# Kernel optimization log

Measured on AMD Instinct MI355X. Metric: run time of the kernel, lower is better.

## Reference

```python
import jax, jax.numpy as jnp
import numpy as np

B, S, E, H = 4, 4096, 512, 64


def setup_inputs() -> dict:
    key = jax.random.key(0)
    ks = jax.random.split(key, 6)
    query = jax.random.normal(ks[0], (B, S, E), dtype=jnp.float32)
    key_t = jax.random.normal(ks[1], (B, S, E), dtype=jnp.float32)
    value = jax.random.normal(ks[2], (B, S, E), dtype=jnp.float32)
    # nn.Linear weights are [out, in] = [H, E]; biases [H]
    Wq = jax.random.normal(ks[3], (H, E), dtype=jnp.float32) * 0.02
    Wk = jax.random.normal(ks[4], (H, E), dtype=jnp.float32) * 0.02
    Wv = jax.random.normal(ks[5], (H, E), dtype=jnp.float32) * 0.02
    bq = jnp.zeros((H,), jnp.float32)
    bk = jnp.zeros((H,), jnp.float32)
    bv = jnp.zeros((H,), jnp.float32)
    # causal mask, broadcast over batch; masked_fill where mask == 0
    mask = jnp.tril(jnp.ones((1, S, S), dtype=jnp.bool_))
    return {"query": query, "key": key_t, "value": value,
            "Wq": Wq, "bq": bq, "Wk": Wk, "bk": bk, "Wv": Wv, "bv": bv,
            "mask": mask}


def reference(query, key, value, Wq, bq, Wk, bk, Wv, bv, mask):
    # Bug-faithful: d_k is the LAST dim of the *input* query, i.e. embed_dim
    d_k = query.shape[-1]
    q = jnp.einsum('bse,he->bsh', query, Wq) + bq   # [B,S,H]
    k = jnp.einsum('bse,he->bsh', key, Wk) + bk     # [B,S,H]
    v = jnp.einsum('bse,he->bsh', value, Wv) + bv   # [B,S,H]
    scores = jnp.einsum('bqh,bkh->bqk', q, k) / jnp.sqrt(jnp.float32(d_k))  # [B,S,S]
    scores = jnp.where(mask, scores, -jnp.inf)
    weights = jax.nn.softmax(scores, axis=-1)
    # dropout_rate = 0.0 -> Dropout is identity
    out = jnp.einsum('bqk,bkh->bqh', weights, v)    # [B,S,H]
    return out
```

## Files before the change

### kernel.cpp

```cpp
#include <hip/hip_runtime.h>
#include <hip/hip_bf16.h>
#include <math.h>

typedef unsigned short u16;
typedef unsigned int   u32;
typedef __attribute__((ext_vector_type(8)))  short bf16x8_t;
typedef __attribute__((ext_vector_type(4)))  float f32x4_t;
typedef __attribute__((ext_vector_type(16))) float f32x16_t;
typedef __attribute__((ext_vector_type(4)))  int   i32x4_t;
typedef __attribute__((ext_vector_type(2)))  u32   u32x2_t;

#define SEQ 4096
#define EMB 512
#define HD  64
#define NBATCH 4
#define C2 0.063758718f

#define NPAIR 136
#define SLOTS (NBATCH * NPAIR * 8)

__device__ __forceinline__ u16 to_bf(float f) {
    __hip_bfloat16 h = __float2bfloat16(f);
    return __builtin_bit_cast(u16, h);
}

__device__ __forceinline__ void stage16(const u16* g, u16* l) {
    __builtin_amdgcn_global_load_lds(
        (const __attribute__((address_space(1))) void*)g,
        (__attribute__((address_space(3))) void*)l, 16, 0, 0);
}

__global__ __launch_bounds__(256)
void proj_kernel(const float* __restrict__ q_in, const float* __restrict__ k_in,
                 const float* __restrict__ v_in,
                 const float* __restrict__ Wq, const float* __restrict__ bq,
                 const float* __restrict__ Wk, const float* __restrict__ bk,
                 const float* __restrict__ Wv, const float* __restrict__ bv,
                 u16* __restrict__ outQ, u16* __restrict__ outK,
                 u16* __restrict__ outVT)
{
    const int z = blockIdx.y;
    const float* in   = (z == 0) ? q_in : (z == 1) ? k_in : v_in;
    const float* W    = (z == 0) ? Wq   : (z == 1) ? Wk   : Wv;
    const float* bias = (z == 0) ? bq   : (z == 1) ? bk   : bv;

    __shared__ u16 A_lds[64][72];
    __shared__ u16 B_lds[64][72];

    const int tid  = threadIdx.x;
    const int lane = tid & 63;
    const int w    = tid >> 6;
    const int l15  = lane & 15;
    const int lg   = lane >> 4;
    const int g0   = blockIdx.x * 64;

    f32x4_t acc[4];
    #pragma unroll
    for (int i = 0; i < 4; ++i)
        #pragma unroll
        for (int j = 0; j < 4; ++j) acc[i][j] = 0.f;

    const int r   = tid >> 2;
    const int seg = tid & 3;

    for (int ec = 0; ec < EMB / 64; ++ec) {
        __syncthreads();
        {
            const float* srcA = in + (size_t)(g0 + r) * EMB + ec * 64 + seg * 16;
            const float* srcB = W  + (size_t)r        * EMB + ec * 64 + seg * 16;
            u16 ta[16], tb[16];
            #pragma unroll
            for (int u = 0; u < 4; ++u) {
                f32x4_t fa = *reinterpret_cast<const f32x4_t*>(srcA + 4 * u);
                f32x4_t fb = *reinterpret_cast<const f32x4_t*>(srcB + 4 * u);
                #pragma unroll
                for (int q = 0; q < 4; ++q) {
                    ta[4 * u + q] = to_bf(fa[q]);
                    tb[4 * u + q] = to_bf(fb[q]);
                }
            }
            *reinterpret_cast<i32x4_t*>(&A_lds[r][seg * 16 + 0]) = *reinterpret_cast<i32x4_t*>(&ta[0]);
            *reinterpret_cast<i32x4_t*>(&A_lds[r][seg * 16 + 8]) = *reinterpret_cast<i32x4_t*>(&ta[8]);
            *reinterpret_cast<i32x4_t*>(&B_lds[r][seg * 16 + 0]) = *reinterpret_cast<i32x4_t*>(&tb[0]);
            *reinterpret_cast<i32x4_t*>(&B_lds[r][seg * 16 + 8]) = *reinterpret_cast<i32x4_t*>(&tb[8]);
        }
        __syncthreads();
        #pragma unroll
        for (int ks = 0; ks < 2; ++ks) {
            bf16x8_t a = *reinterpret_cast<const bf16x8_t*>(&A_lds[w * 16 + l15][ks * 32 + 8 * lg]);
            #pragma unroll
            for (int kn = 0; kn < 4; ++kn) {
                bf16x8_t b = *reinterpret_cast<const bf16x8_t*>(&B_lds[kn * 16 + l15][ks * 32 + 8 * lg]);
                acc[kn] = __builtin_amdgcn_mfma_f32_16x16x32_bf16(a, b, acc[kn], 0, 0, 0);
            }
        }
    }

    #pragma unroll
    for (int kn = 0; kn < 4; ++kn) {
        const int col = kn * 16 + l15;
        const float bb = bias[col];
        #pragma unroll
        for (int j = 0; j < 4; ++j) {
            const int grow = g0 + w * 16 + lg * 4 + j;
            const u16 val = to_bf(acc[kn][j] + bb);
            if (z == 0) {
                outQ[(size_t)grow * HD + col] = val;
            } else if (z == 1) {
                outK[(size_t)grow * HD + col] = val;
            } else {
                const int b = grow >> 12, s = grow & (SEQ - 1);
                outVT[((size_t)(b * HD + col)) * SEQ + s] = val;
            }
        }
    }
}

__global__ __launch_bounds__(512, 4)
void attn8_kernel(const u16* __restrict__ Q, const u16* __restrict__ K,
                  const u16* __restrict__ VT,
                  u16* __restrict__ partO, float* __restrict__ partL)
{
    __shared__ u16 Kt[2][64 * 64];
    __shared__ u16 Vt[2][64 * 64];
    __shared__ u16 Pt[8][32 * 64];

    const int tid  = threadIdx.x;
    const int w    = tid >> 6;
    const int lane = tid & 63;
    const int q31  = lane & 31;
    const int half = lane >> 5;

    const int b = blockIdx.y;
    const int y = blockIdx.x;
    int g = 0;
    while ((g + 1) * (g + 2) / 2 <= y) ++g;
    const int c = y - g * (g + 1) / 2;

    const int R0   = 256 * g + 32 * w;
    const int q_g  = R0 + q31;
    const int nt_w = 4 * g + (w >> 1) + 1;
    const int t0   = 4 * c, t1 = 4 * c + 4;

    const u16* Kb  = K  + (size_t)b * SEQ * HD;
    const u16* VTb = VT + (size_t)b * HD * SEQ;

    const int srow = w * 8 + (lane >> 3);
    const int schk = (lane & 7) ^ ((lane >> 3) & 7);

    bf16x8_t qf0, qf1, qf2, qf3;
    {
        const u16* qp = Q + ((size_t)b * SEQ + q_g) * HD + 8 * half;
        qf0 = *(const bf16x8_t*)(qp + 0);
        qf1 = *(const bf16x8_t*)(qp + 16);
        qf2 = *(const bf16x8_t*)(qp + 32);
        qf3 = *(const bf16x8_t*)(qp + 48);
    }

    f32x16_t acc0, acc1;
    #pragma unroll
    for (int i = 0; i < 16; ++i) { acc0[i] = 0.f; acc1[i] = 0.f; }
    float lsum = 0.f;

    auto STAGE = [&](int u, int t) {
        stage16(&Kb[((size_t)(t * 64 + srow)) * HD + schk * 8], &Kt[u][w * 512]);
        stage16(&VTb[(size_t)srow * SEQ + t * 64 + schk * 8],   &Vt[u][w * 512]);
    };

    STAGE(0, t0);
    asm volatile("s_waitcnt vmcnt(0)" ::: "memory");
    __syncthreads();

    for (int t = t0; t < t1; ++t) {
        const int u = (t - t0) & 1;
        if (t + 1 < t1) STAGE(u ^ 1, t + 1);
        if (t < nt_w) {
            const bool last = (t == nt_w - 1);
            #pragma unroll
            for (int ksub = 0; ksub < 2; ++ksub) {
                f32x16_t sf;
                #pragma unroll
                for (int i = 0; i < 16; ++i) sf[i] = 0.f;
                const int kl = ksub * 32 + q31;
                #pragma unroll
                for (int s = 0; s < 4; ++s) {
                    bf16x8_t a = *(const bf16x8_t*)
                        &Kt[u][kl * 64 + ((s * 16 + 8 * half) ^ ((kl & 7) << 3))];
                    bf16x8_t qq = (s == 0) ? qf0 : (s == 1) ? qf1 : (s == 2) ? qf2 : qf3;
                    sf = __builtin_amdgcn_mfma_f32_32x32x16_bf16(a, qq, sf, 0, 0, 0);
                }
                #pragma unroll
                for (int j = 0; j < 4; ++j) {
                    float p[4];
                    #pragma unroll
                    for (int e = 0; e < 4; ++e) {
                        const int kk    = 8 * j + 4 * half + e;
                        const int key_g = t * 64 + ksub * 32 + kk;
                        float v = exp2f(sf[4 * j + e] * C2);
                        if (last && key_g > q_g) v = 0.f;
                        lsum += v;
                        p[e] = v;
                    }
                    u32x2_t pk;
                    pk[0] = (u32)to_bf(p[0]) | ((u32)to_bf(p[1]) << 16);
                    pk[1] = (u32)to_bf(p[2]) | ((u32)to_bf(p[3]) << 16);
                    const int col = (ksub * 32 + 8 * j + 4 * half) ^ ((q31 & 7) << 3);
                    *(u32x2_t*)&Pt[w][q31 * 64 + col] = pk;
                }
            }
            asm volatile("s_waitcnt lgkmcnt(0)" ::: "memory");
            __builtin_amdgcn_sched_barrier(0);
            #pragma unroll
            for (int kp = 0; kp < 4; ++kp) {
                bf16x8_t pb = *(const bf16x8_t*)
                    &Pt[w][q31 * 64 + ((kp * 16 + 8 * half) ^ ((q31 & 7) << 3))];
                {
                    const int dl = q31;
                    bf16x8_t va = *(const bf16x8_t*)
                        &Vt[u][dl * 64 + ((kp * 16 + 8 * half) ^ ((dl & 7) << 3))];
                    acc0 = __builtin_amdgcn_mfma_f32_32x32x16_bf16(va, pb, acc0, 0, 0, 0);
                }
                {
                    const int dl = 32 + q31;
                    bf16x8_t va = *(const bf16x8_t*)
                        &Vt[u][dl * 64 + ((kp * 16 + 8 * half) ^ ((dl & 7) << 3))];
                    acc1 = __builtin_amdgcn_mfma_f32_32x32x16_bf16(va, pb, acc1, 0, 0, 0);
                }
            }
        }
        asm volatile("s_waitcnt vmcnt(0)" ::: "memory");
        __syncthreads();
    }

    lsum += __shfl_xor(lsum, 32);
    const int slot = (b * NPAIR + y) * 8 + w;
    u16* po = partO + (size_t)slot * 2048;
    #pragma unroll
    for (int dsub = 0; dsub < 2; ++dsub) {
        #pragma unroll
        for (int j = 0; j < 4; ++j) {
            const f32x16_t& a = dsub ? acc1 : acc0;
            u32x2_t pk;
            pk[0] = (u32)to_bf(a[4 * j + 0]) | ((u32)to_bf(a[4 * j + 1]) << 16);
            pk[1] = (u32)to_bf(a[4 * j + 2]) | ((u32)to_bf(a[4 * j + 3]) << 16);
            const int d = 32 * dsub + 8 * j + 4 * half;
            *(u32x2_t*)&po[q31 * 64 + d] = pk;
        }
    }
    if (half == 0) partL[(size_t)slot * 32 + q31] = lsum;
}

__global__ __launch_bounds__(256)
void reduce8_kernel(const u16* __restrict__ partO, const float* __restrict__ partL,
                    float* __restrict__ out)
{
    const int x  = blockIdx.x;
    const int b  = x >> 7;
    const int gw = x & 127;
    const int g  = gw >> 3;
    const int w  = gw & 7;
    const int ybase = g * (g + 1) / 2;

    const int t  = threadIdx.x;
    const int q  = t >> 3;
    const int d0 = (t & 7) * 8;

    float acc[8];
    #pragma unroll
    for (int i = 0; i < 8; ++i) acc[i] = 0.f;
    float l = 0.f;

    for (int c = 0; c <= g; ++c) {
        const int slot = (b * NPAIR + ybase + c) * 8 + w;
        i32x4_t raw = *(const i32x4_t*)(partO + (size_t)slot * 2048 + q * 64 + d0);
        const u16* pr = (const u16*)&raw;
        #pragma unroll
        for (int i = 0; i < 8; ++i) {
            u32 bits = ((u32)pr[i]) << 16;
            acc[i] += __builtin_bit_cast(float, bits);
        }
        l += partL[(size_t)slot * 32 + q];
    }
    const float inv = 1.f / l;
    f32x4_t r0, r1;
    #pragma unroll
    for (int i = 0; i < 4; ++i) { r0[i] = acc[i] * inv; r1[i] = acc[4 + i] * inv; }
    const size_t row = (size_t)b * SEQ + g * 256 + w * 32 + q;
    *(f32x4_t*)&out[row * HD + d0]     = r0;
    *(f32x4_t*)&out[row * HD + d0 + 4] = r1;
}

extern "C" void kernel_launch(void* const* d_in, const int* in_sizes, int n_in,
                              void* d_out, int out_size, void* d_ws, size_t ws_size,
                              hipStream_t stream)
{
    const float* q_in = (const float*)d_in[0];
    const float* k_in = (const float*)d_in[1];
    const float* v_in = (const float*)d_in[2];
    const float* Wq   = (const float*)d_in[3];
    const float* bq   = (const float*)d_in[4];
    const float* Wk   = (const float*)d_in[5];
    const float* bk   = (const float*)d_in[6];
    const float* Wv   = (const float*)d_in[7];
    const float* bv   = (const float*)d_in[8];
    float* out = (float*)d_out;

    const size_t NQ = (size_t)NBATCH * SEQ * HD;
    u16* wsQ   = (u16*)d_ws;
    u16* wsK   = wsQ + NQ;
    u16* wsVT  = wsK + NQ;
    u16* partO = wsVT + NQ;
    float* partL = (float*)(partO + (size_t)SLOTS * 2048);

    proj_kernel<<<dim3(256, 3), 256, 0, stream>>>(q_in, k_in, v_in, Wq, bq, Wk, bk,
                                                  Wv, bv, wsQ, wsK, wsVT);
    attn8_kernel<<<dim3(NPAIR, NBATCH), 512, 0, stream>>>(wsQ, wsK, wsVT, partO, partL);
    reduce8_kernel<<<dim3(512), 256, 0, stream>>>(partO, partL, out);
}
```

Before: 66.83 us.

## Load projection A-operand directly from global into registers, stage only weights in LDS

The projection kernel no longer stages input rows through shared memory. Each lane reads its MFMA A-fragment straight from global memory and converts it to bf16 in registers. Only the weight matrix is staged in LDS, in two 256-wide halves, which cuts barriers from 16 to about 3. The trade-off is less coalesced global reads (each lane reads 32 contiguous bytes per row) and a larger LDS footprint for W.

```diff
diff --git a/kernel.cpp b/kernel.cpp
--- a/kernel.cpp
+++ b/kernel.cpp
@@ -44,8 +44,7 @@
     const float* W    = (z == 0) ? Wq   : (z == 1) ? Wk   : Wv;
     const float* bias = (z == 0) ? bq   : (z == 1) ? bk   : bv;
 
-    __shared__ u16 A_lds[64][72];
-    __shared__ u16 B_lds[64][72];
+    __shared__ u16 W_lds[64][264];
 
     const int tid  = threadIdx.x;
     const int lane = tid & 63;
@@ -54,44 +53,49 @@
     const int lg   = lane >> 4;
     const int g0   = blockIdx.x * 64;
 
+    const float* arow = in + (size_t)(g0 + w * 16 + l15) * EMB + 8 * lg;
+
     f32x4_t acc[4];
     #pragma unroll
     for (int i = 0; i < 4; ++i)
         #pragma unroll
         for (int j = 0; j < 4; ++j) acc[i][j] = 0.f;
 
-    const int r   = tid >> 2;
-    const int seg = tid & 3;
-
-    for (int ec = 0; ec < EMB / 64; ++ec) {
+    const int sr = tid >> 2;
+    const int sc = (tid & 3) * 64;
+
+    #pragma unroll 1
+    for (int half = 0; half < 2; ++half) {
+        if (half) __syncthreads();
+        {
+            const float* src = W + (size_t)sr * EMB + half * 256 + sc;
+            #pragma unroll
+            for (int u = 0; u < 8; ++u) {
+                f32x4_t f0 = *reinterpret_cast<const f32x4_t*>(src + 8 * u);
+                f32x4_t f1 = *reinterpret_cast<const f32x4_t*>(src + 8 * u + 4);
+                u16 tmp[8];
+                #pragma unroll
+                for (int e = 0; e < 4; ++e) { tmp[e] = to_bf(f0[e]); tmp[4 + e] = to_bf(f1[e]); }
+                *reinterpret_cast<i32x4_t*>(&W_lds[sr][sc + 8 * u]) =
+                    *reinterpret_cast<const i32x4_t*>(tmp);
+            }
+        }
         __syncthreads();
-        {
-            const float* srcA = in + (size_t)(g0 + r) * EMB + ec * 64 + seg * 16;
-            const float* srcB = W  + (size_t)r        * EMB + ec * 64 + seg * 16;
-            u16 ta[16], tb[16];
-            #pragma unroll
-            for (int u = 0; u < 4; ++u) {
-                f32x4_t fa = *reinterpret_cast<const f32x4_t*>(srcA + 4 * u);
-                f32x4_t fb = *reinterpret_cast<const f32x4_t*>(srcB + 4 * u);
-                #pragma unroll
-                for (int q = 0; q < 4; ++q) {
-                    ta[4 * u + q] = to_bf(fa[q]);
-                    tb[4 * u + q] = to_bf(fb[q]);
-                }
-            }
-            *reinterpret_cast<i32x4_t*>(&A_lds[r][seg * 16 + 0]) = *reinterpret_cast<i32x4_t*>(&ta[0]);
-            *reinterpret_cast<i32x4_t*>(&A_lds[r][seg * 16 + 8]) = *reinterpret_cast<i32x4_t*>(&ta[8]);
-            *reinterpret_cast<i32x4_t*>(&B_lds[r][seg * 16 + 0]) = *reinterpret_cast<i32x4_t*>(&tb[0]);
-            *reinterpret_cast<i32x4_t*>(&B_lds[r][seg * 16 + 8]) = *reinterpret_cast<i32x4_t*>(&tb[8]);
-        }
-        __syncthreads();
-        #pragma unroll
-        for (int ks = 0; ks < 2; ++ks) {
-            bf16x8_t a = *reinterpret_cast<const bf16x8_t*>(&A_lds[w * 16 + l15][ks * 32 + 8 * lg]);
+
+        const float* abase = arow + half * 256;
+        #pragma unroll 4
+        for (int kt = 0; kt < 8; ++kt) {
+            f32x4_t a0 = *reinterpret_cast<const f32x4_t*>(abase + kt * 32);
+            f32x4_t a1 = *reinterpret_cast<const f32x4_t*>(abase + kt * 32 + 4);
+            u16 ta[8];
+            #pragma unroll
+            for (int e = 0; e < 4; ++e) { ta[e] = to_bf(a0[e]); ta[4 + e] = to_bf(a1[e]); }
+            bf16x8_t af = *reinterpret_cast<const bf16x8_t*>(ta);
             #pragma unroll
             for (int kn = 0; kn < 4; ++kn) {
-                bf16x8_t b = *reinterpret_cast<const bf16x8_t*>(&B_lds[kn * 16 + l15][ks * 32 + 8 * lg]);
-                acc[kn] = __builtin_amdgcn_mfma_f32_16x16x32_bf16(a, b, acc[kn], 0, 0, 0);
+                bf16x8_t bfrag = *reinterpret_cast<const bf16x8_t*>(
+                    &W_lds[kn * 16 + l15][kt * 32 + 8 * lg]);
+                acc[kn] = __builtin_amdgcn_mfma_f32_16x16x32_bf16(af, bfrag, acc[kn], 0, 0, 0);
             }
         }
     }
```

After: 73.85 us. 10.5% more time.
